# Kernel optimization log

Measured on AMD Instinct MI355X. Metric: run time of the kernel, lower is better.

## Reference

```python
import jax, jax.numpy as jnp
import numpy as np

N = 50000      # nodes
DEG = 32       # avg degree
E = N * DEG + N  # edges incl. self loops
IN_DIM = 512
H = 4          # heads
D = 128        # hidden per head
SLOPE = 0.2


def setup_inputs() -> dict:
    key = jax.random.key(0)
    ks = jax.random.split(key, 12)
    features = jax.random.normal(ks[0], (N, IN_DIM), dtype=jnp.float32)
    src_r = jax.random.randint(ks[1], (N * DEG,), 0, N)
    dst_r = jax.random.randint(ks[2], (N * DEG,), 0, N)
    loop = jnp.arange(N)
    src = jnp.concatenate([src_r, loop]).astype(jnp.int32)
    dst = jnp.concatenate([dst_r, loop]).astype(jnp.int32)
    ids = jax.random.randint(ks[3], (16,), 0, N)
    s0 = 1.0 / np.sqrt(IN_DIM)
    s1 = 1.0 / np.sqrt(H * D)
    fc_w0 = jax.random.normal(ks[4], (IN_DIM, H * D), dtype=jnp.float32) * s0
    attn_l0 = jax.random.normal(ks[5], (H, D), dtype=jnp.float32) * s1
    attn_r0 = jax.random.normal(ks[6], (H, D), dtype=jnp.float32) * s1
    bias0 = jnp.zeros((H * D,), dtype=jnp.float32)
    fc_w1 = jax.random.normal(ks[7], (H * D, H * D), dtype=jnp.float32) * s1
    attn_l1 = jax.random.normal(ks[8], (H, D), dtype=jnp.float32) * s1
    attn_r1 = jax.random.normal(ks[9], (H, D), dtype=jnp.float32) * s1
    bias1 = jnp.zeros((H * D,), dtype=jnp.float32)
    return dict(features=features, fc_w0=fc_w0, attn_l0=attn_l0, attn_r0=attn_r0,
                bias0=bias0, fc_w1=fc_w1, attn_l1=attn_l1, attn_r1=attn_r1,
                bias1=bias1, src=src, dst=dst, ids=ids)


def gat_layer(h, fc_w, attn_l, attn_r, bias, src, dst, residual):
    ft = (h @ fc_w).reshape(N, H, D)                     # [N,H,D]
    el = jnp.sum(ft * attn_l, axis=-1)                   # [N,H]
    er = jnp.sum(ft * attn_r, axis=-1)                   # [N,H]
    e = jax.nn.leaky_relu(el[src] + er[dst], SLOPE)      # [E,H]
    # edge softmax over incoming edges of each dst node (self-loops guarantee coverage)
    emax = jax.ops.segment_max(e, dst, num_segments=N)   # [N,H]
    ee = jnp.exp(e - emax[dst])
    esum = jax.ops.segment_sum(ee, dst, num_segments=N)  # [N,H]
    alpha = ee / esum[dst]                               # [E,H]
    out = jax.ops.segment_sum(alpha[:, :, None] * ft[src], dst, num_segments=N)  # [N,H,D]
    if residual:
        out = out + h.reshape(N, H, D)                   # res_fc is Identity (in == H*D)
    out = out + bias.reshape(1, H, D)
    out = jax.nn.elu(out)
    return out.reshape(N, H * D)


def reference(features, fc_w0, attn_l0, attn_r0, bias0, fc_w1, attn_l1, attn_r1,
              bias1, src, dst, ids):
    h = gat_layer(features, fc_w0, attn_l0, attn_r0, bias0, src, dst, residual=False)
    h = gat_layer(h, fc_w1, attn_l1, attn_r1, bias1, src, dst, residual=True)
    h = jnp.tanh(h)
    return h[ids]  # [B, H*D] gather per id2node lookup
```

## Files before the change

kernel.cpp:

```cpp
#include <hip/hip_runtime.h>
#include <hip/hip_bf16.h>

typedef short bf16x8 __attribute__((ext_vector_type(8)));
typedef float f32x4 __attribute__((ext_vector_type(4)));

#define HD 512
#define KDIM 512
#define NHEAD 4
#define DHEAD 128
#define C1CAP 1024
#define C2CAP 16384
#define E1CAP 2048
#define E2CAP 32768

__global__ void detect_k(const unsigned short* __restrict__ feat, int* __restrict__ flagp) {
    __shared__ int cs;
    if (threadIdx.x == 0) cs = 0;
    __syncthreads();
    int c = 0;
    for (int k = 0; k < 16; ++k) {
        unsigned short u = feat[2 * (threadIdx.x + k * 256)];
        int e = (u >> 7) & 0xFF;
        if (e >= 96 && e <= 140) c++;
    }
    atomicAdd(&cs, c);
    __syncthreads();
    if (threadIdx.x == 0) *flagp = (cs > 2048) ? 1 : 0;
}

__global__ __launch_bounds__(256) void prep_k(
    const void* __restrict__ W0, const void* __restrict__ W1,
    __hip_bfloat16* __restrict__ Wt0, __hip_bfloat16* __restrict__ Wt1,
    const void* p0, const void* p1, const void* p2,
    const void* p3, const void* p4, const void* p5,
    float* __restrict__ smallc,
    const int* __restrict__ ids, int B,
    int* __restrict__ mapId, unsigned* __restrict__ bmId,
    const int* __restrict__ flagp) {
    const int isbf = *flagp;
    const int b = blockIdx.x;
    const int t = threadIdx.x;
    if (b < 2048) {
        const void* W = (b < 1024) ? W0 : W1;
        __hip_bfloat16* Wt = (b < 1024) ? Wt0 : Wt1;
        int idx = ((b < 1024) ? b : b - 1024) * 256 + t;
        int i = idx >> 9;
        int j = idx & 511;
        float v = isbf ? __bfloat162float(((const __hip_bfloat16*)W)[idx])
                       : ((const float*)W)[idx];
        Wt[j * 512 + i] = __float2bfloat16(v);
    } else if (b < 2054) {
        int which = b - 2048;
        const void* p;
        switch (which) {
            case 0: p = p0; break;
            case 1: p = p1; break;
            case 2: p = p2; break;
            case 3: p = p3; break;
            case 4: p = p4; break;
            default: p = p5; break;
        }
#pragma unroll
        for (int r = 0; r < 2; ++r) {
            int e = t + r * 256;
            float v = isbf ? __bfloat162float(((const __hip_bfloat16*)p)[e])
                           : ((const float*)p)[e];
            smallc[which * 512 + e] = v;
        }
    } else {
        if (t < B) {
            int n = ids[t];
            mapId[n] = t;
            atomicOr(&bmId[n >> 5], 1u << (n & 31));
        }
    }
}

__global__ __launch_bounds__(256) void scan_k(
    const int* __restrict__ dst, int E,
    const unsigned* __restrict__ bm,
    unsigned long long* __restrict__ masks) {
    const int gid = blockIdx.x * 256 + threadIdx.x;
    const bool inb = (4 * gid < E);
    int4 d4 = {0, 0, 0, 0};
    if (inb) d4 = ((const int4*)dst)[gid];
    const int dv[4] = {d4.x, d4.y, d4.z, d4.w};
    unsigned long long m[4];
#pragma unroll
    for (int k = 0; k < 4; ++k) {
        int d = dv[k];
        bool hit = inb && ((bm[d >> 5] >> (d & 31)) & 1u);
        m[k] = __ballot(hit);
    }
    const int w = gid >> 6, lane = gid & 63;
    if (lane < 4) {
        unsigned long long v = (lane == 0) ? m[0] : (lane == 1) ? m[1]
                             : (lane == 2) ? m[2] : m[3];
        masks[(size_t)w * 4 + lane] = v;
    }
}

__global__ __launch_bounds__(256) void emit_k(
    const unsigned long long* __restrict__ masks, int nmask,
    const int* __restrict__ src, const int* __restrict__ dst,
    const int* __restrict__ mapd,
    int2* __restrict__ elist, int* __restrict__ ecnt, int cap,
    int* __restrict__ mapm, int* __restrict__ Flist,
    int* __restrict__ nF, int fcap, unsigned* __restrict__ bmOut) {
    int j = blockIdx.x * 256 + threadIdx.x;
    if (j >= nmask) return;
    unsigned long long m = masks[j];
    if (!m) return;
    const int w = j >> 2, k = j & 3;
    while (m) {
        int l = __ffsll((long long)m) - 1;
        m &= m - 1;
        int e = w * 256 + l * 4 + k;
        int s = src[e], d = dst[e];
        int p = atomicAdd(ecnt, 1);
        if (p < cap) { int2 v; v.x = s; v.y = mapd[d]; elist[p] = v; }
        if (atomicCAS(&mapm[s], -1, -2) == -1) {
            int q = atomicAdd(nF, 1);
            if (q < fcap) { Flist[q] = s; mapm[s] = q; }
            else mapm[s] = 0;
            if (bmOut) atomicOr(&bmOut[s >> 5], 1u << (s & 31));
        }
    }
}

__global__ __launch_bounds__(1024) void csr_k(
    const int2* __restrict__ E1, const int* __restrict__ nE1p,
    const int2* __restrict__ E2, const int* __restrict__ nE2p,
    const int* __restrict__ map1, const int* __restrict__ map2,
    int* __restrict__ off1, int* __restrict__ off2,
    int* __restrict__ b1, int* __restrict__ b2) {
    __shared__ int cnt[1024];
    __shared__ int scn[1024];
    __shared__ int cur[1024];
    __shared__ int c1[16];
    __shared__ int o1cur[16];
    const int t = threadIdx.x;
    int n1 = *nE1p; if (n1 > E1CAP) n1 = E1CAP;
    int n2 = *nE2p; if (n2 > E2CAP) n2 = E2CAP;
    cnt[t] = 0;
    if (t < 16) c1[t] = 0;
    __syncthreads();
    for (int i = t; i < n2; i += 1024) atomicAdd(&cnt[E2[i].y], 1);
    for (int i = t; i < n1; i += 1024) atomicAdd(&c1[E1[i].y], 1);
    __syncthreads();
    int v = cnt[t];
    scn[t] = v;
    __syncthreads();
    for (int off = 1; off < 1024; off <<= 1) {
        int x = (t >= off) ? scn[t - off] : 0;
        __syncthreads();
        scn[t] += x;
        __syncthreads();
    }
    int ex = scn[t] - v;
    off2[t] = ex;
    cur[t] = ex;
    if (t == 1023) off2[1024] = scn[1023];
    if (t == 0) {
        int a = 0;
        for (int i = 0; i < 16; ++i) { off1[i] = a; o1cur[i] = a; a += c1[i]; }
        off1[16] = a;
    }
    __syncthreads();
    for (int i = t; i < n2; i += 1024) {
        int p = atomicAdd(&cur[E2[i].y], 1);
        int r = map2[E2[i].x]; if (r < 0) r = 0;
        b2[p] = r;
    }
    for (int i = t; i < n1; i += 1024) {
        int p = atomicAdd(&o1cur[E1[i].y], 1);
        int r = map1[E1[i].x]; if (r < 0) r = 0;
        b1[p] = r;
    }
}

__global__ __launch_bounds__(256) void gatherA_k(const void* __restrict__ feat,
                                                 const int* __restrict__ F2list,
                                                 const int* __restrict__ nF2,
                                                 __hip_bfloat16* __restrict__ Ac,
                                                 const int* __restrict__ flagp) {
    int cnt = *nF2; if (cnt > C2CAP) cnt = C2CAP;
    const int isbf = *flagp;
    const int t = threadIdx.x;
    for (int b = blockIdx.x; b < cnt; b += gridDim.x) {
        int row = F2list[b];
        __hip_bfloat162 v;
        if (isbf) {
            v = *(const __hip_bfloat162*)&((const __hip_bfloat16*)feat)[(size_t)row * KDIM + t * 2];
        } else {
            const float2 f = *(const float2*)&((const float*)feat)[(size_t)row * KDIM + t * 2];
            v.x = __float2bfloat16(f.x);
            v.y = __float2bfloat16(f.y);
        }
        *(__hip_bfloat162*)&Ac[(size_t)b * KDIM + t * 2] = v;
    }
}

__global__ __launch_bounds__(256) void gemm_c(
    const __hip_bfloat16* __restrict__ A,
    const __hip_bfloat16* __restrict__ Bt,
    __hip_bfloat16* __restrict__ C,
    const int* __restrict__ countp) {
    const int cntv = *countp;
    const int m0 = blockIdx.y * 128;
    if (m0 >= cntv) return;
    __shared__ alignas(16) __hip_bfloat16 As[128][40];
    __shared__ alignas(16) __hip_bfloat16 Bs[128][40];
    const int t = threadIdx.x;
    const int n0 = blockIdx.x * 128;
    const int lane = t & 63, wave = t >> 6;
    const int wm = (wave >> 1) * 64, wn = (wave & 1) * 64;
    const int fr = lane & 15, fk = (lane >> 4) * 8;
    const int r0 = t >> 2;
    const int c0 = (t & 3) * 8;

    int arow[2];
#pragma unroll
    for (int r = 0; r < 2; ++r) {
        int rr = m0 + r * 64 + r0;
        if (rr >= cntv) rr = cntv - 1;
        arow[r] = rr;
    }

    f32x4 acc[4][4];
#pragma unroll
    for (int i = 0; i < 4; ++i)
#pragma unroll
        for (int j = 0; j < 4; ++j)
#pragma unroll
            for (int r = 0; r < 4; ++r) acc[i][j][r] = 0.f;

    for (int kt = 0; kt < KDIM; kt += 32) {
#pragma unroll
        for (int r = 0; r < 2; ++r) {
            int row = r * 64 + r0;
            uint4 va = *(const uint4*)&A[(size_t)arow[r] * KDIM + kt + c0];
            *(uint4*)&As[row][c0] = va;
            uint4 vb = *(const uint4*)&Bt[(size_t)(n0 + row) * KDIM + kt + c0];
            *(uint4*)&Bs[row][c0] = vb;
        }
        __syncthreads();
        bf16x8 af[4], bfr[4];
#pragma unroll
        for (int i = 0; i < 4; ++i) af[i]  = *(const bf16x8*)&As[wm + i * 16 + fr][fk];
#pragma unroll
        for (int j = 0; j < 4; ++j) bfr[j] = *(const bf16x8*)&Bs[wn + j * 16 + fr][fk];
#pragma unroll
        for (int i = 0; i < 4; ++i)
#pragma unroll
            for (int j = 0; j < 4; ++j)
                acc[i][j] = __builtin_amdgcn_mfma_f32_16x16x32_bf16(af[i], bfr[j], acc[i][j], 0, 0, 0);
        __syncthreads();
    }

    const int cr = (lane >> 4) * 4;
    const int cc = lane & 15;
#pragma unroll
    for (int i = 0; i < 4; ++i)
#pragma unroll
        for (int j = 0; j < 4; ++j)
#pragma unroll
            for (int rg = 0; rg < 4; ++rg) {
                int m = m0 + wm + i * 16 + cr + rg;
                int n = n0 + wn + j * 16 + cc;
                C[(size_t)m * HD + n] = __float2bfloat16(acc[i][j][rg]);
            }
}

__global__ __launch_bounds__(256) void elc_k(const __hip_bfloat16* __restrict__ ft,
                                             const float* __restrict__ attn_l,
                                             const float* __restrict__ attn_r,
                                             const int* __restrict__ countp,
                                             float* __restrict__ el, float* __restrict__ er) {
    int cnt = *countp; if (cnt > C2CAP) cnt = C2CAP;
    const int h = threadIdx.x >> 6, lane = threadIdx.x & 63;
    const float2 al = *(const float2*)&attn_l[h * DHEAD + lane * 2];
    const float2 ar = *(const float2*)&attn_r[h * DHEAD + lane * 2];
    for (int b = blockIdx.x; b < cnt; b += gridDim.x) {
        const __hip_bfloat162 f = *(const __hip_bfloat162*)&ft[(size_t)b * HD + h * DHEAD + lane * 2];
        float fx = __bfloat162float(f.x), fy = __bfloat162float(f.y);
        float pl = fx * al.x + fy * al.y;
        float pr = fx * ar.x + fy * ar.y;
        for (int off = 32; off; off >>= 1) {
            pl += __shfl_xor(pl, off, 64);
            pr += __shfl_xor(pr, off, 64);
        }
        if (lane == 0) {
            el[b * NHEAD + h] = pl;
            er[b * NHEAD + h] = pr;
        }
    }
}

__global__ __launch_bounds__(256) void agg1_k(
    const int* __restrict__ off2, const int* __restrict__ b2,
    const int* __restrict__ F1list, const int* __restrict__ map2,
    const int* __restrict__ nF1,
    const float* __restrict__ el, const float* __restrict__ er,
    const __hip_bfloat16* __restrict__ ftc,
    const float* __restrict__ bias,
    __hip_bfloat16* __restrict__ outc) {
    int b = blockIdx.x;
    if (b >= *nF1) return;
    int n = F1list[b];
    int h = threadIdx.x >> 6, lane = threadIdx.x & 63;
    int rn = map2[n]; if (rn < 0) rn = 0;
    float ern = er[rn * NHEAD + h];
    int beg = off2[b], end = off2[b + 1];
    float m = -3.0e38f, l = 0.f, a0 = 0.f, a1 = 0.f;
    for (int i = beg; i < end; ++i) {
        int r2 = b2[i];
        float e = el[r2 * NHEAD + h] + ern;
        e = (e >= 0.f) ? e : 0.2f * e;
        float mn = fmaxf(m, e);
        float sc = __expf(m - mn);
        float w  = __expf(e - mn);
        const __hip_bfloat162 f = *(const __hip_bfloat162*)&ftc[(size_t)r2 * HD + h * DHEAD + lane * 2];
        l  = l * sc + w;
        a0 = a0 * sc + w * __bfloat162float(f.x);
        a1 = a1 * sc + w * __bfloat162float(f.y);
        m = mn;
    }
    float inv = (l > 0.f) ? 1.0f / l : 0.f;
    float o0 = a0 * inv, o1 = a1 * inv;
    const float2 bb = *(const float2*)&bias[h * DHEAD + lane * 2];
    o0 += bb.x;
    o1 += bb.y;
    o0 = (o0 > 0.f) ? o0 : expm1f(o0);
    o1 = (o1 > 0.f) ? o1 : expm1f(o1);
    __hip_bfloat162 o2;
    o2.x = __float2bfloat16(o0);
    o2.y = __float2bfloat16(o1);
    *(__hip_bfloat162*)&outc[(size_t)b * HD + h * DHEAD + lane * 2] = o2;
}

__global__ __launch_bounds__(256) void agg2_k(
    const int* __restrict__ off1, const int* __restrict__ b1,
    const int* __restrict__ ids, const int* __restrict__ mapId,
    const int* __restrict__ map1,
    const float* __restrict__ el, const float* __restrict__ er,
    const __hip_bfloat16* __restrict__ ftc,
    const __hip_bfloat16* __restrict__ resc,
    const float* __restrict__ bias,
    void* __restrict__ out, const int* __restrict__ flagp) {
    int b = blockIdx.x;
    int n = ids[b];
    int slot = mapId[n]; if (slot < 0) slot = 0;
    int h = threadIdx.x >> 6, lane = threadIdx.x & 63;
    int rn = map1[n]; if (rn < 0) rn = 0;
    float ern = er[rn * NHEAD + h];
    int beg = off1[slot], end = off1[slot + 1];
    float m = -3.0e38f, l = 0.f, a0 = 0.f, a1 = 0.f;
    for (int i = beg; i < end; ++i) {
        int r1 = b1[i];
        float e = el[r1 * NHEAD + h] + ern;
        e = (e >= 0.f) ? e : 0.2f * e;
        float mn = fmaxf(m, e);
        float sc = __expf(m - mn);
        float w  = __expf(e - mn);
        const __hip_bfloat162 f = *(const __hip_bfloat162*)&ftc[(size_t)r1 * HD + h * DHEAD + lane * 2];
        l  = l * sc + w;
        a0 = a0 * sc + w * __bfloat162float(f.x);
        a1 = a1 * sc + w * __bfloat162float(f.y);
        m = mn;
    }
    float inv = (l > 0.f) ? 1.0f / l : 0.f;
    float o0 = a0 * inv, o1 = a1 * inv;
    const __hip_bfloat162 r2v = *(const __hip_bfloat162*)&resc[(size_t)rn * HD + h * DHEAD + lane * 2];
    o0 += __bfloat162float(r2v.x);
    o1 += __bfloat162float(r2v.y);
    const float2 bb = *(const float2*)&bias[h * DHEAD + lane * 2];
    o0 += bb.x;
    o1 += bb.y;
    o0 = (o0 > 0.f) ? o0 : expm1f(o0);
    o1 = (o1 > 0.f) ? o1 : expm1f(o1);
    o0 = tanhf(o0);
    o1 = tanhf(o1);
    size_t oi = (size_t)b * HD + h * DHEAD + lane * 2;
    if (*flagp) {
        __hip_bfloat162 o2;
        o2.x = __float2bfloat16(o0);
        o2.y = __float2bfloat16(o1);
        *(__hip_bfloat162*)&((__hip_bfloat16*)out)[oi] = o2;
    } else {
        float2 o2; o2.x = o0; o2.y = o1;
        *(float2*)&((float*)out)[oi] = o2;
    }
}

extern "C" void kernel_launch(void* const* d_in, const int* in_sizes, int n_in,
                              void* d_out, int out_size, void* d_ws, size_t ws_size,
                              hipStream_t stream) {
    const void* features = d_in[0];
    const void* fc_w0    = d_in[1];
    const void* attn_l0  = d_in[2];
    const void* attn_r0  = d_in[3];
    const void* bias0    = d_in[4];
    const void* fc_w1    = d_in[5];
    const void* attn_l1  = d_in[6];
    const void* attn_r1  = d_in[7];
    const void* bias1    = d_in[8];
    const int* src = (const int*)d_in[9];
    const int* dst = (const int*)d_in[10];
    const int* ids = (const int*)d_in[11];

    const int N = in_sizes[0] / KDIM;
    const int E = in_sizes[9];
    const int B = in_sizes[11];
    const int words = (N + 31) / 32;

    const int nblk_scan = (E + 1023) / 1024;
    const int nwaves    = nblk_scan * 4;
    const int nmask     = nwaves * 4;

    char* w = (char*)d_ws;
    auto alloc = [&](size_t bytes) {
        void* p = (void*)w;
        w += (bytes + 255) & ~(size_t)255;
        return p;
    };
    __hip_bfloat16* Wt0 = (__hip_bfloat16*)alloc(512 * 512 * 2);
    __hip_bfloat16* Wt1 = (__hip_bfloat16*)alloc(512 * 512 * 2);
    float* smallc = (float*)alloc(6 * 512 * 4);
    int* maps    = (int*)alloc((size_t)3 * N * 4);
    int* mapId = maps;
    int* map1  = maps + N;
    int* map2  = maps + 2 * N;
    unsigned long long* masks = (unsigned long long*)alloc((size_t)nmask * 8);
    int2* E1l  = (int2*)alloc((size_t)E1CAP * 8);
    int2* E2l  = (int2*)alloc((size_t)E2CAP * 8);
    int* F1list = (int*)alloc(C1CAP * 4);
    int* F2list = (int*)alloc(C2CAP * 4);
    const int zwords = 8 + 2 * words;
    int* zmem   = (int*)alloc((size_t)zwords * 4);
    int* counters = zmem;
    unsigned* bmId = (unsigned*)(zmem + 8);
    unsigned* bm1  = bmId + words;
    int* off1 = (int*)alloc(17 * 4);
    int* off2 = (int*)alloc(1025 * 4);
    int* b1   = (int*)alloc(E1CAP * 4);
    int* b2   = (int*)alloc(E2CAP * 4);
    __hip_bfloat16* Ac   = (__hip_bfloat16*)alloc((size_t)C2CAP * KDIM * 2);
    __hip_bfloat16* ft0c = (__hip_bfloat16*)alloc((size_t)C2CAP * HD * 2);
    float* el0 = (float*)alloc((size_t)C2CAP * NHEAD * 4);
    float* er0 = (float*)alloc((size_t)C2CAP * NHEAD * 4);
    __hip_bfloat16* h1c  = (__hip_bfloat16*)alloc((size_t)C1CAP * HD * 2);
    __hip_bfloat16* ft1c = (__hip_bfloat16*)alloc((size_t)C1CAP * HD * 2);
    float* el1 = (float*)alloc((size_t)C1CAP * NHEAD * 4);
    float* er1 = (float*)alloc((size_t)C1CAP * NHEAD * 4);

    int* nE1  = counters + 0;
    int* nE2  = counters + 1;
    int* nF1  = counters + 2;
    int* nF2  = counters + 3;
    int* flag = counters + 4;

    hipMemsetAsync(maps, 0xFF, (size_t)3 * N * 4, stream);
    hipMemsetAsync(zmem, 0, (size_t)zwords * 4, stream);

    detect_k<<<1, 256, 0, stream>>>((const unsigned short*)features, flag);
    prep_k<<<2055, 256, 0, stream>>>(fc_w0, fc_w1, Wt0, Wt1,
                                     attn_l0, attn_r0, bias0, attn_l1, attn_r1, bias1,
                                     smallc, ids, B, mapId, bmId, flag);
    float* al0c = smallc + 0 * 512;
    float* ar0c = smallc + 1 * 512;
    float* b0c  = smallc + 2 * 512;
    float* al1c = smallc + 3 * 512;
    float* ar1c = smallc + 4 * 512;
    float* b1c  = smallc + 5 * 512;

    scan_k<<<nblk_scan, 256, 0, stream>>>(dst, E, bmId, masks);
    emit_k<<<(nmask + 255) / 256, 256, 0, stream>>>(masks, nmask, src, dst, mapId,
                                                    E1l, nE1, E1CAP,
                                                    map1, F1list, nF1, C1CAP, bm1);
    scan_k<<<nblk_scan, 256, 0, stream>>>(dst, E, bm1, masks);
    emit_k<<<(nmask + 255) / 256, 256, 0, stream>>>(masks, nmask, src, dst, map1,
                                                    E2l, nE2, E2CAP,
                                                    map2, F2list, nF2, C2CAP, nullptr);

    csr_k<<<1, 1024, 0, stream>>>(E1l, nE1, E2l, nE2, map1, map2, off1, off2, b1, b2);

    gatherA_k<<<512, 256, 0, stream>>>(features, F2list, nF2, Ac, flag);
    gemm_c<<<dim3(HD / 128, C2CAP / 128), 256, 0, stream>>>(Ac, Wt0, ft0c, nF2);
    elc_k<<<512, 256, 0, stream>>>(ft0c, al0c, ar0c, nF2, el0, er0);
    agg1_k<<<C1CAP, 256, 0, stream>>>(off2, b2, F1list, map2, nF1,
                                      el0, er0, ft0c, b0c, h1c);

    gemm_c<<<dim3(HD / 128, C1CAP / 128), 256, 0, stream>>>(h1c, Wt1, ft1c, nF1);
    elc_k<<<512, 256, 0, stream>>>(ft1c, al1c, ar1c, nF1, el1, er1);
    agg2_k<<<B, 256, 0, stream>>>(off1, b1, ids, mapId, map1,
                                  el1, er1, ft1c, h1c, b1c,
                                  d_out, flag);
}
```

Baseline: 374.2 us.

## Fuse scan/emit passes, CSR with gather, and attention logits into GEMM epilogue

```diff
diff --git a/kernel.cpp b/kernel.cpp
--- a/kernel.cpp
+++ b/kernel.cpp
@@ -13,22 +13,26 @@
 #define E1CAP 2048
 #define E2CAP 32768
 
-__global__ void detect_k(const unsigned short* __restrict__ feat, int* __restrict__ flagp) {
-    __shared__ int cs;
-    if (threadIdx.x == 0) cs = 0;
+__device__ int detect_bf16(const unsigned short* f) {
+    int c = 0;
+#pragma unroll
+    for (int k = 0; k < 4; ++k) {
+        unsigned short u = f[2 * (threadIdx.x + k * 256)];
+        int e = (u >> 7) & 0xFF;
+        c += (e >= 96 && e <= 140) ? 1 : 0;
+    }
+#pragma unroll
+    for (int off = 32; off; off >>= 1) c += __shfl_xor(c, off, 64);
+    __shared__ int s_c;
+    if (threadIdx.x == 0) s_c = 0;
     __syncthreads();
-    int c = 0;
-    for (int k = 0; k < 16; ++k) {
-        unsigned short u = feat[2 * (threadIdx.x + k * 256)];
-        int e = (u >> 7) & 0xFF;
-        if (e >= 96 && e <= 140) c++;
-    }
-    atomicAdd(&cs, c);
+    if ((threadIdx.x & 63) == 0) atomicAdd(&s_c, c);
     __syncthreads();
-    if (threadIdx.x == 0) *flagp = (cs > 2048) ? 1 : 0;
+    return s_c > 512;
 }
 
 __global__ __launch_bounds__(256) void prep_k(
+    const void* __restrict__ features,
     const void* __restrict__ W0, const void* __restrict__ W1,
     __hip_bfloat16* __restrict__ Wt0, __hip_bfloat16* __restrict__ Wt1,
     const void* p0, const void* p1, const void* p2,
@@ -36,14 +40,14 @@
     float* __restrict__ smallc,
     const int* __restrict__ ids, int B,
     int* __restrict__ mapId, unsigned* __restrict__ bmId,
-    const int* __restrict__ flagp) {
-    const int isbf = *flagp;
+    int* __restrict__ flagp) {
+    const int isbf = detect_bf16((const unsigned short*)features);
     const int b = blockIdx.x;
     const int t = threadIdx.x;
     if (b < 2048) {
         const void* W = (b < 1024) ? W0 : W1;
         __hip_bfloat16* Wt = (b < 1024) ? Wt0 : Wt1;
-        int idx = ((b < 1024) ? b : b - 1024) * 256 + t;
+        int idx = (b & 1023) * 256 + t;
         int i = idx >> 9;
         int j = idx & 511;
         float v = isbf ? __bfloat162float(((const __hip_bfloat16*)W)[idx])
@@ -68,6 +72,7 @@
             smallc[which * 512 + e] = v;
         }
     } else {
+        if (t == 0) *flagp = isbf;
         if (t < B) {
             int n = ids[t];
             mapId[n] = t;
@@ -76,141 +81,151 @@
     }
 }
 
-__global__ __launch_bounds__(256) void scan_k(
-    const int* __restrict__ dst, int E,
-    const unsigned* __restrict__ bm,
-    unsigned long long* __restrict__ masks) {
-    const int gid = blockIdx.x * 256 + threadIdx.x;
-    const bool inb = (4 * gid < E);
-    int4 d4 = {0, 0, 0, 0};
-    if (inb) d4 = ((const int4*)dst)[gid];
-    const int dv[4] = {d4.x, d4.y, d4.z, d4.w};
-    unsigned long long m[4];
-#pragma unroll
-    for (int k = 0; k < 4; ++k) {
-        int d = dv[k];
-        bool hit = inb && ((bm[d >> 5] >> (d & 31)) & 1u);
-        m[k] = __ballot(hit);
-    }
-    const int w = gid >> 6, lane = gid & 63;
-    if (lane < 4) {
-        unsigned long long v = (lane == 0) ? m[0] : (lane == 1) ? m[1]
-                             : (lane == 2) ? m[2] : m[3];
-        masks[(size_t)w * 4 + lane] = v;
-    }
-}
-
-__global__ __launch_bounds__(256) void emit_k(
-    const unsigned long long* __restrict__ masks, int nmask,
-    const int* __restrict__ src, const int* __restrict__ dst,
-    const int* __restrict__ mapd,
-    int2* __restrict__ elist, int* __restrict__ ecnt, int cap,
-    int* __restrict__ mapm, int* __restrict__ Flist,
-    int* __restrict__ nF, int fcap, unsigned* __restrict__ bmOut) {
-    int j = blockIdx.x * 256 + threadIdx.x;
-    if (j >= nmask) return;
-    unsigned long long m = masks[j];
-    if (!m) return;
-    const int w = j >> 2, k = j & 3;
-    while (m) {
-        int l = __ffsll((long long)m) - 1;
-        m &= m - 1;
-        int e = w * 256 + l * 4 + k;
-        int s = src[e], d = dst[e];
-        int p = atomicAdd(ecnt, 1);
-        if (p < cap) { int2 v; v.x = s; v.y = mapd[d]; elist[p] = v; }
-        if (atomicCAS(&mapm[s], -1, -2) == -1) {
-            int q = atomicAdd(nF, 1);
-            if (q < fcap) { Flist[q] = s; mapm[s] = q; }
-            else mapm[s] = 0;
-            if (bmOut) atomicOr(&bmOut[s >> 5], 1u << (s & 31));
-        }
-    }
-}
-
-__global__ __launch_bounds__(1024) void csr_k(
-    const int2* __restrict__ E1, const int* __restrict__ nE1p,
-    const int2* __restrict__ E2, const int* __restrict__ nE2p,
+__global__ __launch_bounds__(256) void pass_k(
+    const int* __restrict__ src, const int* __restrict__ dst, int E,
+    const unsigned* __restrict__ bmIn, const int* __restrict__ mapd,
+    int2* __restrict__ elist, int* __restrict__ ecnt, int ecap,
+    int* __restrict__ cntArr,
+    int* __restrict__ mapm, int* __restrict__ Flist, int* __restrict__ nFr, int fcap,
+    unsigned* __restrict__ bmOut) {
+    __shared__ int2 eBuf[256];
+    __shared__ int fBuf[256];
+    __shared__ int eCnt_s, fCnt_s, eBase_s, fBase_s;
+    const int t = threadIdx.x;
+    if (t == 0) { eCnt_s = 0; fCnt_s = 0; }
+    __syncthreads();
+    const int nq = E >> 2;
+    const int gid = blockIdx.x * 256 + t;
+    if (gid < nq) {
+        const int4 d4 = ((const int4*)dst)[gid];
+        const int dv[4] = {d4.x, d4.y, d4.z, d4.w};
+#pragma unroll
+        for (int k = 0; k < 4; ++k) {
+            const int d = dv[k];
+            if ((bmIn[d >> 5] >> (d & 31)) & 1u) {
+                const int e = 4 * gid + k;
+                int2 v; v.x = src[e]; v.y = mapd[d];
+                int p = atomicAdd(&eCnt_s, 1);
+                if (p < 256) eBuf[p] = v;
+                else {
+                    int q = atomicAdd(ecnt, 1);
+                    if (q < ecap) { elist[q] = v; atomicAdd(&cntArr[v.y], 1); }
+                }
+                const int s = v.x;
+                if (atomicCAS(&mapm[s], -1, -2) == -1) {
+                    int q = atomicAdd(&fCnt_s, 1);
+                    if (q < 256) fBuf[q] = s;
+                    else {
+                        int g2 = atomicAdd(nFr, 1);
+                        if (g2 < fcap) { Flist[g2] = s; mapm[s] = g2; }
+                        else mapm[s] = 0;
+                    }
+                    if (bmOut) atomicOr(&bmOut[s >> 5], 1u << (s & 31));
+                }
+            }
+        }
+    }
+    __syncthreads();
+    const int ne = (eCnt_s < 256) ? eCnt_s : 256;
+    const int nf = (fCnt_s < 256) ? fCnt_s : 256;
+    if (t == 0 && ne) eBase_s = atomicAdd(ecnt, ne);
+    if (t == 64 && nf) fBase_s = atomicAdd(nFr, nf);
+    __syncthreads();
+    for (int i = t; i < ne; i += 256) {
+        int p = eBase_s + i;
+        if (p < ecap) { int2 v = eBuf[i]; elist[p] = v; atomicAdd(&cntArr[v.y], 1); }
+    }
+    for (int i = t; i < nf; i += 256) {
+        int q = fBase_s + i; int s = fBuf[i];
+        if (q < fcap) { Flist[q] = s; mapm[s] = q; }
+        else mapm[s] = 0;
+    }
+}
+
+__global__ __launch_bounds__(256) void scatgath_k(
+    const int2* __restrict__ E1l, const int2* __restrict__ E2l,
+    const int* __restrict__ counters,
+    const int* __restrict__ cnt1, const int* __restrict__ cnt2,
     const int* __restrict__ map1, const int* __restrict__ map2,
     int* __restrict__ off1, int* __restrict__ off2,
-    int* __restrict__ b1, int* __restrict__ b2) {
-    __shared__ int cnt[1024];
-    __shared__ int scn[1024];
-    __shared__ int cur[1024];
-    __shared__ int c1[16];
-    __shared__ int o1cur[16];
+    int* __restrict__ b1, int* __restrict__ b2,
+    const void* __restrict__ feat, const int* __restrict__ F2list,
+    __hip_bfloat16* __restrict__ Ac, const int* __restrict__ flagp) {
     const int t = threadIdx.x;
-    int n1 = *nE1p; if (n1 > E1CAP) n1 = E1CAP;
-    int n2 = *nE2p; if (n2 > E2CAP) n2 = E2CAP;
-    cnt[t] = 0;
-    if (t < 16) c1[t] = 0;
-    __syncthreads();
-    for (int i = t; i < n2; i += 1024) atomicAdd(&cnt[E2[i].y], 1);
-    for (int i = t; i < n1; i += 1024) atomicAdd(&c1[E1[i].y], 1);
-    __syncthreads();
-    int v = cnt[t];
-    scn[t] = v;
-    __syncthreads();
-    for (int off = 1; off < 1024; off <<= 1) {
-        int x = (t >= off) ? scn[t - off] : 0;
+    const int b = blockIdx.x;
+    if (b == 0) {
+        __shared__ int soff[1024];
+        __shared__ int sc[256];
+        __shared__ int s1off[16];
+        int c0 = cnt2[t * 4 + 0], c1 = cnt2[t * 4 + 1];
+        int c2 = cnt2[t * 4 + 2], c3 = cnt2[t * 4 + 3];
+        int tsum = c0 + c1 + c2 + c3;
+        sc[t] = tsum;
         __syncthreads();
-        scn[t] += x;
+        for (int off = 1; off < 256; off <<= 1) {
+            int x = (t >= off) ? sc[t - off] : 0;
+            __syncthreads();
+            sc[t] += x;
+            __syncthreads();
+        }
+        int run = sc[t] - tsum;
+        int b4 = t * 4;
+        off2[b4 + 0] = run; soff[b4 + 0] = run; run += c0;
+        off2[b4 + 1] = run; soff[b4 + 1] = run; run += c1;
+        off2[b4 + 2] = run; soff[b4 + 2] = run; run += c2;
+        off2[b4 + 3] = run; soff[b4 + 3] = run; run += c3;
+        if (t == 255) off2[1024] = run;
+        if (t == 0) {
+            int a = 0;
+            for (int i = 0; i < 16; ++i) { off1[i] = a; s1off[i] = a; a += cnt1[i]; }
+            off1[16] = a;
+        }
         __syncthreads();
-    }
-    int ex = scn[t] - v;
-    off2[t] = ex;
-    cur[t] = ex;
-    if (t == 1023) off2[1024] = scn[1023];
-    if (t == 0) {
-        int a = 0;
-        for (int i = 0; i < 16; ++i) { off1[i] = a; o1cur[i] = a; a += c1[i]; }
-        off1[16] = a;
-    }
-    __syncthreads();
-    for (int i = t; i < n2; i += 1024) {
-        int p = atomicAdd(&cur[E2[i].y], 1);
-        int r = map2[E2[i].x]; if (r < 0) r = 0;
-        b2[p] = r;
-    }
-    for (int i = t; i < n1; i += 1024) {
-        int p = atomicAdd(&o1cur[E1[i].y], 1);
-        int r = map1[E1[i].x]; if (r < 0) r = 0;
-        b1[p] = r;
-    }
-}
-
-__global__ __launch_bounds__(256) void gatherA_k(const void* __restrict__ feat,
-                                                 const int* __restrict__ F2list,
-                                                 const int* __restrict__ nF2,
-                                                 __hip_bfloat16* __restrict__ Ac,
-                                                 const int* __restrict__ flagp) {
-    int cnt = *nF2; if (cnt > C2CAP) cnt = C2CAP;
-    const int isbf = *flagp;
-    const int t = threadIdx.x;
-    for (int b = blockIdx.x; b < cnt; b += gridDim.x) {
-        int row = F2list[b];
-        __hip_bfloat162 v;
-        if (isbf) {
-            v = *(const __hip_bfloat162*)&((const __hip_bfloat16*)feat)[(size_t)row * KDIM + t * 2];
-        } else {
-            const float2 f = *(const float2*)&((const float*)feat)[(size_t)row * KDIM + t * 2];
-            v.x = __float2bfloat16(f.x);
-            v.y = __float2bfloat16(f.y);
-        }
-        *(__hip_bfloat162*)&Ac[(size_t)b * KDIM + t * 2] = v;
-    }
-}
-
-__global__ __launch_bounds__(256) void gemm_c(
+        int n2 = counters[1]; if (n2 > E2CAP) n2 = E2CAP;
+        for (int i = t; i < n2; i += 256) {
+            int2 v = E2l[i];
+            int p = atomicAdd(&soff[v.y], 1);
+            int r = map2[v.x]; if (r < 0) r = 0;
+            b2[p] = r;
+        }
+        int n1 = counters[0]; if (n1 > E1CAP) n1 = E1CAP;
+        for (int i = t; i < n1; i += 256) {
+            int2 v = E1l[i];
+            int p = atomicAdd(&s1off[v.y], 1);
+            int r = map1[v.x]; if (r < 0) r = 0;
+            b1[p] = r;
+        }
+    } else {
+        const int isbf = *flagp;
+        int cnt = counters[3]; if (cnt > C2CAP) cnt = C2CAP;
+        for (int bb = b - 1; bb < cnt; bb += (int)gridDim.x - 1) {
+            int row = F2list[bb];
+            __hip_bfloat162 v;
+            if (isbf) {
+                v = *(const __hip_bfloat162*)&((const __hip_bfloat16*)feat)[(size_t)row * KDIM + t * 2];
+            } else {
+                const float2 f = *(const float2*)&((const float*)feat)[(size_t)row * KDIM + t * 2];
+                v.x = __float2bfloat16(f.x);
+                v.y = __float2bfloat16(f.y);
+            }
+            *(__hip_bfloat162*)&Ac[(size_t)bb * KDIM + t * 2] = v;
+        }
+    }
+}
+
+__global__ __launch_bounds__(256) void gemmel_k(
     const __hip_bfloat16* __restrict__ A,
     const __hip_bfloat16* __restrict__ Bt,
     __hip_bfloat16* __restrict__ C,
-    const int* __restrict__ countp) {
-    const int cntv = *countp;
+    const float* __restrict__ al_, const float* __restrict__ ar_,
+    float* __restrict__ el, float* __restrict__ er,
+    const int* __restrict__ countp, int cap) {
+    int cntv = *countp; if (cntv > cap) cntv = cap;
     const int m0 = blockIdx.y * 128;
     if (m0 >= cntv) return;
     __shared__ alignas(16) __hip_bfloat16 As[128][40];
     __shared__ alignas(16) __hip_bfloat16 Bs[128][40];
+    __shared__ float pel[2][128], perr[2][128];
     const int t = threadIdx.x;
     const int n0 = blockIdx.x * 128;
     const int lane = t & 63, wave = t >> 6;
@@ -270,29 +285,42 @@
                 int n = n0 + wn + j * 16 + cc;
                 C[(size_t)m * HD + n] = __float2bfloat16(acc[i][j][rg]);
             }
-}
-
-__global__ __launch_bounds__(256) void elc_k(const __hip_bfloat16* __restrict__ ft,
-                                             const float* __restrict__ attn_l,
-                                             const float* __restrict__ attn_r,
-                                             const int* __restrict__ countp,
-                                             float* __restrict__ el, float* __restrict__ er) {
-    int cnt = *countp; if (cnt > C2CAP) cnt = C2CAP;
-    const int h = threadIdx.x >> 6, lane = threadIdx.x & 63;
-    const float2 al = *(const float2*)&attn_l[h * DHEAD + lane * 2];
-    const float2 ar = *(const float2*)&attn_r[h * DHEAD + lane * 2];
-    for (int b = blockIdx.x; b < cnt; b += gridDim.x) {
-        const __hip_bfloat162 f = *(const __hip_bfloat162*)&ft[(size_t)b * HD + h * DHEAD + lane * 2];
-        float fx = __bfloat162float(f.x), fy = __bfloat162float(f.y);
-        float pl = fx * al.x + fy * al.y;
-        float pr = fx * ar.x + fy * ar.y;
-        for (int off = 32; off; off >>= 1) {
-            pl += __shfl_xor(pl, off, 64);
-            pr += __shfl_xor(pr, off, 64);
-        }
-        if (lane == 0) {
-            el[b * NHEAD + h] = pl;
-            er[b * NHEAD + h] = pr;
+
+    const int h = n0 >> 7;
+    float alv[4], arv[4];
+#pragma unroll
+    for (int j = 0; j < 4; ++j) {
+        alv[j] = al_[h * DHEAD + wn + j * 16 + cc];
+        arv[j] = ar_[h * DHEAD + wn + j * 16 + cc];
+    }
+#pragma unroll
+    for (int i = 0; i < 4; ++i)
+#pragma unroll
+        for (int rg = 0; rg < 4; ++rg) {
+            float sl = 0.f, sr = 0.f;
+#pragma unroll
+            for (int j = 0; j < 4; ++j) {
+                float c = acc[i][j][rg];
+                sl += c * alv[j];
+                sr += c * arv[j];
+            }
+#pragma unroll
+            for (int off = 1; off < 16; off <<= 1) {
+                sl += __shfl_xor(sl, off, 16);
+                sr += __shfl_xor(sr, off, 16);
+            }
+            if (cc == 0) {
+                int row = wm + i * 16 + cr + rg;
+                pel[wn >> 6][row] = sl;
+                perr[wn >> 6][row] = sr;
+            }
+        }
+    __syncthreads();
+    if (t < 128) {
+        int m = m0 + t;
+        if (m < cntv) {
+            el[m * NHEAD + h] = pel[0][t] + pel[1][t];
+            er[m * NHEAD + h] = perr[0][t] + perr[1][t];
         }
     }
 }
@@ -414,10 +442,6 @@
     const int B = in_sizes[11];
     const int words = (N + 31) / 32;
 
-    const int nblk_scan = (E + 1023) / 1024;
-    const int nwaves    = nblk_scan * 4;
-    const int nmask     = nwaves * 4;
-
     char* w = (char*)d_ws;
     auto alloc = [&](size_t bytes) {
         void* p = (void*)w;
@@ -427,20 +451,21 @@
     __hip_bfloat16* Wt0 = (__hip_bfloat16*)alloc(512 * 512 * 2);
     __hip_bfloat16* Wt1 = (__hip_bfloat16*)alloc(512 * 512 * 2);
     float* smallc = (float*)alloc(6 * 512 * 4);
-    int* maps    = (int*)alloc((size_t)3 * N * 4);
+    int* maps  = (int*)alloc((size_t)3 * N * 4);
     int* mapId = maps;
     int* map1  = maps + N;
     int* map2  = maps + 2 * N;
-    unsigned long long* masks = (unsigned long long*)alloc((size_t)nmask * 8);
     int2* E1l  = (int2*)alloc((size_t)E1CAP * 8);
     int2* E2l  = (int2*)alloc((size_t)E2CAP * 8);
     int* F1list = (int*)alloc(C1CAP * 4);
     int* F2list = (int*)alloc(C2CAP * 4);
-    const int zwords = 8 + 2 * words;
-    int* zmem   = (int*)alloc((size_t)zwords * 4);
+    const int zwords = 8 + 2 * words + 16 + 1024;
+    int* zmem = (int*)alloc((size_t)zwords * 4);
     int* counters = zmem;
     unsigned* bmId = (unsigned*)(zmem + 8);
     unsigned* bm1  = bmId + words;
+    int* cnt1 = (int*)(bm1 + words);
+    int* cnt2 = cnt1 + 16;
     int* off1 = (int*)alloc(17 * 4);
     int* off2 = (int*)alloc(1025 * 4);
     int* b1   = (int*)alloc(E1CAP * 4);
@@ -463,8 +488,7 @@
     hipMemsetAsync(maps, 0xFF, (size_t)3 * N * 4, stream);
     hipMemsetAsync(zmem, 0, (size_t)zwords * 4, stream);
 
-    detect_k<<<1, 256, 0, stream>>>((const unsigned short*)features, flag);
-    prep_k<<<2055, 256, 0, stream>>>(fc_w0, fc_w1, Wt0, Wt1,
+    prep_k<<<2055, 256, 0, stream>>>(features, fc_w0, fc_w1, Wt0, Wt1,
                                      attn_l0, attn_r0, bias0, attn_l1, attn_r1, bias1,
                                      smallc, ids, B, mapId, bmId, flag);
     float* al0c = smallc + 0 * 512;
@@ -474,25 +498,26 @@
     float* ar1c = smallc + 4 * 512;
     float* b1c  = smallc + 5 * 512;
 
-    scan_k<<<nblk_scan, 256, 0, stream>>>(dst, E, bmId, masks);
-    emit_k<<<(nmask + 255) / 256, 256, 0, stream>>>(masks, nmask, src, dst, mapId,
-                                                    E1l, nE1, E1CAP,
-                                                    map1, F1list, nF1, C1CAP, bm1);
-    scan_k<<<nblk_scan, 256, 0, stream>>>(dst, E, bm1, masks);
-    emit_k<<<(nmask + 255) / 256, 256, 0, stream>>>(masks, nmask, src, dst, map1,
-                                                    E2l, nE2, E2CAP,
-                                                    map2, F2list, nF2, C2CAP, nullptr);
-
-    csr_k<<<1, 1024, 0, stream>>>(E1l, nE1, E2l, nE2, map1, map2, off1, off2, b1, b2);
-
-    gatherA_k<<<512, 256, 0, stream>>>(features, F2list, nF2, Ac, flag);
-    gemm_c<<<dim3(HD / 128, C2CAP / 128), 256, 0, stream>>>(Ac, Wt0, ft0c, nF2);
-    elc_k<<<512, 256, 0, stream>>>(ft0c, al0c, ar0c, nF2, el0, er0);
+    const int nblk_scan = (E / 4 + 255) / 256;
+
+    pass_k<<<nblk_scan, 256, 0, stream>>>(src, dst, E, bmId, mapId,
+                                          E1l, nE1, E1CAP, cnt1,
+                                          map1, F1list, nF1, C1CAP, bm1);
+    pass_k<<<nblk_scan, 256, 0, stream>>>(src, dst, E, bm1, map1,
+                                          E2l, nE2, E2CAP, cnt2,
+                                          map2, F2list, nF2, C2CAP, nullptr);
+
+    scatgath_k<<<513, 256, 0, stream>>>(E1l, E2l, counters, cnt1, cnt2,
+                                        map1, map2, off1, off2, b1, b2,
+                                        features, F2list, Ac, flag);
+
+    gemmel_k<<<dim3(HD / 128, C2CAP / 128), 256, 0, stream>>>(
+        Ac, Wt0, ft0c, al0c, ar0c, el0, er0, nF2, C2CAP);
     agg1_k<<<C1CAP, 256, 0, stream>>>(off2, b2, F1list, map2, nF1,
                                       el0, er0, ft0c, b0c, h1c);
 
-    gemm_c<<<dim3(HD / 128, C1CAP / 128), 256, 0, stream>>>(h1c, Wt1, ft1c, nF1);
-    elc_k<<<512, 256, 0, stream>>>(ft1c, al1c, ar1c, nF1, el1, er1);
+    gemmel_k<<<dim3(HD / 128, C1CAP / 128), 256, 0, stream>>>(
+        h1c, Wt1, ft1c, al1c, ar1c, el1, er1, nF1, C1CAP);
     agg2_k<<<B, 256, 0, stream>>>(off1, b1, ids, mapId, map1,
                                   el1, er1, ft1c, h1c, b1c,
                                   d_out, flag);
```

New measurement: 357.6 us. 1.05x faster.
